# Optimization experiments

Measured on AMD Instinct MI355X. Metric: run time of the kernel, lower is better.

Reference implementation:

```python
import jax, jax.numpy as jnp
import numpy as np

B, D, K = 64, 8732, 81
RATIO = 1.0

def setup_inputs() -> dict:
    key = jax.random.key(0)
    k1, k2, k3, k4 = jax.random.split(key, 4)
    return {
        'loc_preds': jax.random.normal(k1, (B, D, 4), dtype=jnp.float32),
        'loc_targets': jax.random.normal(k2, (B, D, 4), dtype=jnp.float32),
        'conf_preds': jax.random.normal(k3, (B, D, K), dtype=jnp.float32),
        'conf_targets': jax.random.randint(k4, (B, D), 0, K, dtype=jnp.int32),
    }

def reference(loc_preds, loc_targets, conf_preds, conf_targets):
    b, d, k = conf_preds.shape
    pos = conf_targets > 0                                  # [B, D] bool
    num_matched = jnp.sum(pos).astype(conf_preds.dtype)     # scalar (python float in torch)
    num_matched = jax.lax.stop_gradient(num_matched)

    # --- localization smooth-L1 over positive boxes only ---
    z = jnp.abs(loc_preds - loc_targets)
    sl1 = jnp.where(z < 1.0, 0.5 * z * z, z - 0.5)          # [B, D, 4]
    loc_loss = jnp.sum(sl1 * pos[..., None].astype(sl1.dtype))

    # --- per-box CE (custom: GLOBAL max for stability), detached, for mining ---
    x = conf_preds.reshape(-1, k)                           # [B*D, K]
    y = conf_targets.reshape(-1)                            # [B*D]
    xmax = jnp.max(x)                                       # x.data.max() in torch (global scalar)
    lse = jnp.log(jnp.sum(jnp.exp(x - xmax), axis=1)) + xmax
    ce_mine = lse - jnp.take_along_axis(x, y[:, None].astype(jnp.int32), axis=1)[:, 0]
    conf_loss_mat = jax.lax.stop_gradient(ce_mine).reshape(b, d)

    # --- hard negative mining: double argsort rank trick ---
    cl = jnp.where(pos, 0.0, conf_loss_mat)                 # conf_loss[pos] = 0
    idx = jnp.argsort(-cl, axis=1)                          # descending sort indices
    rank = jnp.argsort(idx, axis=1)                         # rank of each box
    num_pos = jnp.sum(pos, axis=1, keepdims=True).astype(jnp.float32)   # [B,1]
    num_neg = jnp.minimum(3.0 * RATIO * num_pos, float(d - 1))          # clamp max=D-1
    neg = rank.astype(jnp.float32) < num_neg                # [B, D] bool

    # --- final confidence loss: standard CE summed over pos | neg ---
    sel = (pos | neg).reshape(-1)                           # [B*D]
    logp = jax.nn.log_softmax(x, axis=1)
    ce = -jnp.take_along_axis(logp, y[:, None].astype(jnp.int32), axis=1)[:, 0]
    conf_loss = jnp.sum(jnp.where(sel, ce, 0.0))

    loc_loss = loc_loss / num_matched
    conf_loss = conf_loss / num_matched
    return (loc_loss + conf_loss, conf_loss, loc_loss)
```

## Files before the change

### kernel.cpp

```cpp
#include <hip/hip_runtime.h>
#include <math.h>

constexpr int BB = 64;
constexpr int DD = 8732;
constexpr int KK = 81;
constexpr int SL = 137;
constexpr int NCHUNK = BB * SL;
constexpr int NPART = NCHUNK;
constexpr int NBLKS = 2048;

typedef float f4 __attribute__((ext_vector_type(4)));

__device__ inline float smooth_l1(float d) {
    float z = fabsf(d);
    return z < 1.0f ? 0.5f * z * z : z - 0.5f;
}

__global__ void __launch_bounds__(256) fused_kernel(
    const f4* __restrict__ lp, const f4* __restrict__ lt,
    const float* __restrict__ cp, const int* __restrict__ ct,
    int* __restrict__ cnt_part, float* __restrict__ ce_part,
    float* __restrict__ loc_part)
{
    int tid = threadIdx.x;
    int q = tid & 3, grp = tid >> 2;
    int lane = tid & 63, wid = tid >> 6;
    __shared__ float s_l[4], s_e[4];
    __shared__ int   s_c[4];

    for (int c = blockIdx.x; c < NCHUNK; c += NBLKS) {
        int row = c / SL, sl = c - row * SL;
        int bir = sl * 64 + grp;
        float ce_c = 0.0f, locs = 0.0f;
        int cc = 0;
        if (bir < DD) {
            size_t g = (size_t)row * DD + bir;
            const float* rowp = cp + g * KK;
            const f4* r4 = (const f4*)rowp;
            f4 f[5];
            #pragma unroll
            for (int t = 0; t < 5; ++t) f[t] = r4[q + 4 * t];

            float s = 0.0f;
            #pragma unroll
            for (int t = 0; t < 5; ++t)
                s += __expf(f[t].x) + __expf(f[t].y)
                   + __expf(f[t].z) + __expf(f[t].w);
            if (q == 0) s += __expf(rowp[80]);
            s += __shfl_xor(s, 1);
            s += __shfl_xor(s, 2);

            int y = ct[g];
            float xv = rowp[y];
            if (q == 0) ce_c = __logf(s) - xv;
            if (q == 1 && y > 0) {
                cc = 1;
                f4 a = lp[g], b = lt[g];
                locs = smooth_l1(a.x - b.x) + smooth_l1(a.y - b.y)
                     + smooth_l1(a.z - b.z) + smooth_l1(a.w - b.w);
            }
        }
        for (int o = 32; o; o >>= 1) {
            locs += __shfl_down(locs, o);
            ce_c += __shfl_down(ce_c, o);
            cc   += __shfl_down(cc, o);
        }
        if (c != blockIdx.x) __syncthreads();
        if (lane == 0) { s_l[wid] = locs; s_e[wid] = ce_c; s_c[wid] = cc; }
        __syncthreads();
        if (tid == 0) {
            loc_part[c] = s_l[0] + s_l[1] + s_l[2] + s_l[3];
            ce_part[c]  = s_e[0] + s_e[1] + s_e[2] + s_e[3];
            cnt_part[c] = s_c[0] + s_c[1] + s_c[2] + s_c[3];
        }
    }
}

__global__ void __launch_bounds__(1024) finish_kernel(
    const int* __restrict__ cnt_part, const float* __restrict__ ce_part,
    const float* __restrict__ loc_part, const float* __restrict__ cp,
    const int* __restrict__ ct, float* __restrict__ out)
{
    __shared__ int s_np[BB];
    __shared__ double s_ce[BB];
    __shared__ double s_l[16], s_n[16], s_fs[16];
    __shared__ double s_conf;
    __shared__ int s_fb[BB], s_nfb;
    __shared__ float cl[DD];

    int tid = threadIdx.x;
    int lane = tid & 63, wid = tid >> 6;
    int row = tid >> 4, sub = tid & 15;

    int np = 0; double ces = 0.0;
    for (int s = sub; s < SL; s += 16) {
        int idx = row * SL + s;
        np += cnt_part[idx];
        ces += (double)ce_part[idx];
    }
    for (int o = 8; o; o >>= 1) { np += __shfl_down(np, o); ces += __shfl_down(ces, o); }
    if (sub == 0) { s_np[row] = np; s_ce[row] = ces; }

    double l = 0.0, n = 0.0;
    for (int j = tid; j < NPART; j += 1024) {
        l += (double)loc_part[j];
        n += (double)cnt_part[j];
    }
    for (int o = 32; o; o >>= 1) { l += __shfl_down(l, o); n += __shfl_down(n, o); }
    if (lane == 0) { s_l[wid] = l; s_n[wid] = n; }
    __syncthreads();

    if (tid == 0) {
        double conf = 0.0; int nfb = 0;
        for (int r = 0; r < BB; ++r) {
            float numneg = fminf(3.0f * (float)s_np[r], (float)(DD - 1));
            int M = DD - s_np[r];
            if ((float)M <= numneg) conf += s_ce[r];
            else s_fb[nfb++] = r;
        }
        s_conf = conf; s_nfb = nfb;
    }
    __syncthreads();

    for (int fi = 0; fi < s_nfb; ++fi) {
        int r = s_fb[fi];
        float numneg = fminf(3.0f * (float)s_np[r], (float)(DD - 1));
        const int* ctr = ct + r * DD;
        const float* base = cp + (size_t)r * DD * KK;
        double sum = 0.0;
        for (int i = tid; i < DD; i += 1024) {
            const float* rowp = base + (size_t)i * KK;
            float m = -INFINITY;
            for (int k = 0; k < KK; ++k) m = fmaxf(m, rowp[k]);
            float s = 0.0f;
            for (int k = 0; k < KK; ++k) s += __expf(rowp[k] - m);
            float cei = __logf(s) + m - rowp[ctr[i]];
            if (ctr[i] > 0) { sum += (double)cei; cl[i] = 0.0f; }
            else cl[i] = cei;
        }
        __syncthreads();
        for (int i = tid; i < DD; i += 1024) {
            if (ctr[i] > 0) continue;
            float ci = cl[i];
            int rk = 0;
            for (int j = 0; j < DD; j++) {
                float cj = cl[j];
                rk += (cj > ci || (cj == ci && j < i)) ? 1 : 0;
            }
            if ((float)rk < numneg) sum += (double)ci;
        }
        for (int o = 32; o; o >>= 1) sum += __shfl_down(sum, o);
        if (lane == 0) s_fs[wid] = sum;
        __syncthreads();
        if (tid == 0) {
            double t = 0.0;
            for (int k = 0; k < 16; ++k) t += s_fs[k];
            s_conf += t;
        }
        __syncthreads();
    }

    if (tid == 0) {
        double L = 0.0, N = 0.0;
        for (int k = 0; k < 16; ++k) { L += s_l[k]; N += s_n[k]; }
        double C = s_conf;
        out[0] = (float)(L / N + C / N);
        out[1] = (float)(C / N);
        out[2] = (float)(L / N);
    }
}

extern "C" void kernel_launch(void* const* d_in, const int* in_sizes, int n_in,
                              void* d_out, int out_size, void* d_ws, size_t ws_size,
                              hipStream_t stream) {
    const f4* lp = (const f4*)d_in[0];
    const f4* lt = (const f4*)d_in[1];
    const float* cp = (const float*)d_in[2];
    const int* ct = (const int*)d_in[3];
    float* out = (float*)d_out;

    char* w = (char*)d_ws;
    int*   cnt_part = (int*)w;
    float* loc_part = (float*)(w + 35072);
    float* ce_part  = (float*)(w + 70144);

    fused_kernel<<<NBLKS, 256, 0, stream>>>(lp, lt, cp, ct,
                                            cnt_part, ce_part, loc_part);
    finish_kernel<<<1, 1024, 0, stream>>>(cnt_part, ce_part, loc_part, cp, ct, out);
}
```

Before: 51.68 us.

## Stream conf_preds as flat 64-byte lines per thread with shared-memory box reduction

The main kernel now treats each block's 192 boxes as a contiguous span of floats. Each of up to 972 threads loads one 16-float aligned line with four vector loads, computes exps, and atomically adds partial sums into per-box shared accumulators, also picking out the target logit. This replaces the prior 4-threads-per-box strided row access, which issued misaligned loads (81-float rows) plus a scalar tail and gather, with fully coalesced aligned loads. Because blocks can straddle batch rows, per-block partials are split into two segments that the finish kernel folds into per-row sums with shared atomics. The cost is extra LDS atomics, a float instead of double per-row CE accumulation, and a large 1024-thread block size.

```diff
diff --git a/kernel.cpp b/kernel.cpp
--- a/kernel.cpp
+++ b/kernel.cpp
@@ -4,10 +4,10 @@
 constexpr int BB = 64;
 constexpr int DD = 8732;
 constexpr int KK = 81;
-constexpr int SL = 137;
-constexpr int NCHUNK = BB * SL;
-constexpr int NPART = NCHUNK;
-constexpr int NBLKS = 2048;
+constexpr int NBOX = BB * DD;
+constexpr int BXB = 192;
+constexpr int DWB = BXB * KK;
+constexpr int NBLK = (NBOX + BXB - 1) / BXB;
 
 typedef float f4 __attribute__((ext_vector_type(4)));
 
@@ -16,95 +16,115 @@
     return z < 1.0f ? 0.5f * z * z : z - 0.5f;
 }
 
-__global__ void __launch_bounds__(256) fused_kernel(
+__global__ void __launch_bounds__(1024) fused_kernel(
     const f4* __restrict__ lp, const f4* __restrict__ lt,
     const float* __restrict__ cp, const int* __restrict__ ct,
-    int* __restrict__ cnt_part, float* __restrict__ ce_part,
-    float* __restrict__ loc_part)
+    int* __restrict__ cntA, float* __restrict__ ceA,
+    int* __restrict__ cntB, float* __restrict__ ceB,
+    float* __restrict__ locP)
 {
-    int tid = threadIdx.x;
-    int q = tid & 3, grp = tid >> 2;
+    __shared__ float bsum[BXB];
+    __shared__ float bxv[BXB];
+    __shared__ int   bct[BXB];
+    __shared__ float reA[16], reB[16], rl[16];
+    __shared__ int   rcA[16], rcB[16];
+
+    int tid = threadIdx.x, blk = blockIdx.x;
+    int g0 = blk * BXB;
+    int nb = min(BXB, NBOX - g0);
+    int nlines = nb * KK / 16;
+
+    if (tid < nb) { bct[tid] = ct[g0 + tid]; bsum[tid] = 0.0f; }
+    __syncthreads();
+
+    if (tid < nlines) {
+        size_t d0 = (size_t)blk * DWB + (size_t)tid * 16;
+        const f4* p = (const f4*)(cp + d0);
+        f4 a0 = p[0], a1 = p[1], a2 = p[2], a3 = p[3];
+        int lb  = (tid * 16) / KK;
+        int rem = tid * 16 - lb * KK;
+        int k = KK - rem; if (k > 16) k = 16;
+        float v[16] = { a0.x, a0.y, a0.z, a0.w, a1.x, a1.y, a1.z, a1.w,
+                        a2.x, a2.y, a2.z, a2.w, a3.x, a3.y, a3.z, a3.w };
+        int jt0 = bct[lb] - rem;
+        int jt1 = 1000;
+        if (k < 16) jt1 = k + bct[lb + 1];
+        float xv0 = 0.0f, xv1 = 0.0f, s0 = 0.0f, s1 = 0.0f;
+        #pragma unroll
+        for (int j = 0; j < 16; ++j) {
+            float vj = v[j];
+            if (j == jt0) xv0 = vj;
+            if (j == jt1) xv1 = vj;
+            float e = __expf(vj);
+            if (j < k) s0 += e; else s1 += e;
+        }
+        atomicAdd(&bsum[lb], s0);
+        if ((unsigned)jt0 < 16u) bxv[lb] = xv0;
+        if (k < 16) {
+            atomicAdd(&bsum[lb + 1], s1);
+            if (jt1 < 16) bxv[lb + 1] = xv1;
+        }
+    }
+    __syncthreads();
+
+    float ce = 0.0f, loc = 0.0f; int cnt = 0, seg = 0;
+    if (tid < nb) {
+        int g = g0 + tid;
+        int y = bct[tid];
+        ce = __logf(bsum[tid]) - bxv[tid];
+        seg = (g / DD) - (g0 / DD);
+        if (y > 0) {
+            cnt = 1;
+            f4 A = lp[g], Bv = lt[g];
+            loc = smooth_l1(A.x - Bv.x) + smooth_l1(A.y - Bv.y)
+                + smooth_l1(A.z - Bv.z) + smooth_l1(A.w - Bv.w);
+        }
+    }
+    float ceAv = seg ? 0.0f : ce, ceBv = seg ? ce : 0.0f;
+    int   cAv  = seg ? 0 : cnt,  cBv  = seg ? cnt : 0;
+    for (int o = 32; o; o >>= 1) {
+        ceAv += __shfl_down(ceAv, o); ceBv += __shfl_down(ceBv, o);
+        cAv  += __shfl_down(cAv,  o); cBv  += __shfl_down(cBv,  o);
+        loc  += __shfl_down(loc,  o);
+    }
     int lane = tid & 63, wid = tid >> 6;
-    __shared__ float s_l[4], s_e[4];
-    __shared__ int   s_c[4];
-
-    for (int c = blockIdx.x; c < NCHUNK; c += NBLKS) {
-        int row = c / SL, sl = c - row * SL;
-        int bir = sl * 64 + grp;
-        float ce_c = 0.0f, locs = 0.0f;
-        int cc = 0;
-        if (bir < DD) {
-            size_t g = (size_t)row * DD + bir;
-            const float* rowp = cp + g * KK;
-            const f4* r4 = (const f4*)rowp;
-            f4 f[5];
-            #pragma unroll
-            for (int t = 0; t < 5; ++t) f[t] = r4[q + 4 * t];
-
-            float s = 0.0f;
-            #pragma unroll
-            for (int t = 0; t < 5; ++t)
-                s += __expf(f[t].x) + __expf(f[t].y)
-                   + __expf(f[t].z) + __expf(f[t].w);
-            if (q == 0) s += __expf(rowp[80]);
-            s += __shfl_xor(s, 1);
-            s += __shfl_xor(s, 2);
-
-            int y = ct[g];
-            float xv = rowp[y];
-            if (q == 0) ce_c = __logf(s) - xv;
-            if (q == 1 && y > 0) {
-                cc = 1;
-                f4 a = lp[g], b = lt[g];
-                locs = smooth_l1(a.x - b.x) + smooth_l1(a.y - b.y)
-                     + smooth_l1(a.z - b.z) + smooth_l1(a.w - b.w);
-            }
-        }
-        for (int o = 32; o; o >>= 1) {
-            locs += __shfl_down(locs, o);
-            ce_c += __shfl_down(ce_c, o);
-            cc   += __shfl_down(cc, o);
-        }
-        if (c != blockIdx.x) __syncthreads();
-        if (lane == 0) { s_l[wid] = locs; s_e[wid] = ce_c; s_c[wid] = cc; }
-        __syncthreads();
-        if (tid == 0) {
-            loc_part[c] = s_l[0] + s_l[1] + s_l[2] + s_l[3];
-            ce_part[c]  = s_e[0] + s_e[1] + s_e[2] + s_e[3];
-            cnt_part[c] = s_c[0] + s_c[1] + s_c[2] + s_c[3];
-        }
+    if (lane == 0) { reA[wid]=ceAv; reB[wid]=ceBv; rcA[wid]=cAv; rcB[wid]=cBv; rl[wid]=loc; }
+    __syncthreads();
+    if (tid == 0) {
+        float eA = 0, eB = 0, L = 0; int cA = 0, cB = 0;
+        #pragma unroll
+        for (int w = 0; w < 16; ++w) { eA+=reA[w]; eB+=reB[w]; cA+=rcA[w]; cB+=rcB[w]; L+=rl[w]; }
+        ceA[blk] = eA; ceB[blk] = eB; cntA[blk] = cA; cntB[blk] = cB; locP[blk] = L;
     }
 }
 
 __global__ void __launch_bounds__(1024) finish_kernel(
-    const int* __restrict__ cnt_part, const float* __restrict__ ce_part,
-    const float* __restrict__ loc_part, const float* __restrict__ cp,
+    const int* __restrict__ cntA, const float* __restrict__ ceA,
+    const int* __restrict__ cntB, const float* __restrict__ ceB,
+    const float* __restrict__ locP, const float* __restrict__ cp,
     const int* __restrict__ ct, float* __restrict__ out)
 {
-    __shared__ int s_np[BB];
-    __shared__ double s_ce[BB];
+    __shared__ int   s_np[BB];
+    __shared__ float s_cef[BB];
     __shared__ double s_l[16], s_n[16], s_fs[16];
     __shared__ double s_conf;
     __shared__ int s_fb[BB], s_nfb;
     __shared__ float cl[DD];
 
-    int tid = threadIdx.x;
-    int lane = tid & 63, wid = tid >> 6;
-    int row = tid >> 4, sub = tid & 15;
-
-    int np = 0; double ces = 0.0;
-    for (int s = sub; s < SL; s += 16) {
-        int idx = row * SL + s;
-        np += cnt_part[idx];
-        ces += (double)ce_part[idx];
-    }
-    for (int o = 8; o; o >>= 1) { np += __shfl_down(np, o); ces += __shfl_down(ces, o); }
-    if (sub == 0) { s_np[row] = np; s_ce[row] = ces; }
+    int tid = threadIdx.x, lane = tid & 63, wid = tid >> 6;
+    if (tid < BB) { s_np[tid] = 0; s_cef[tid] = 0.0f; }
+    __syncthreads();
 
     double l = 0.0, n = 0.0;
-    for (int j = tid; j < NPART; j += 1024) {
-        l += (double)loc_part[j];
-        n += (double)cnt_part[j];
+    for (int e = tid; e < NBLK; e += 1024) {
+        int rA = (e * BXB) / DD;
+        int ca = cntA[e], cb = cntB[e];
+        float ea = ceA[e], eb = ceB[e];
+        atomicAdd(&s_np[rA], ca);
+        atomicAdd(&s_cef[rA], ea);
+        if (rA + 1 < BB) { atomicAdd(&s_np[rA + 1], cb); atomicAdd(&s_cef[rA + 1], eb); }
+        l += (double)locP[e];
+        n += (double)(ca + cb);
     }
     for (int o = 32; o; o >>= 1) { l += __shfl_down(l, o); n += __shfl_down(n, o); }
     if (lane == 0) { s_l[wid] = l; s_n[wid] = n; }
@@ -115,7 +135,7 @@
         for (int r = 0; r < BB; ++r) {
             float numneg = fminf(3.0f * (float)s_np[r], (float)(DD - 1));
             int M = DD - s_np[r];
-            if ((float)M <= numneg) conf += s_ce[r];
+            if ((float)M <= numneg) conf += (double)s_cef[r];
             else s_fb[nfb++] = r;
         }
         s_conf = conf; s_nfb = nfb;
@@ -131,9 +151,9 @@
         for (int i = tid; i < DD; i += 1024) {
             const float* rowp = base + (size_t)i * KK;
             float m = -INFINITY;
-            for (int k = 0; k < KK; ++k) m = fmaxf(m, rowp[k]);
+            for (int kk = 0; kk < KK; ++kk) m = fmaxf(m, rowp[kk]);
             float s = 0.0f;
-            for (int k = 0; k < KK; ++k) s += __expf(rowp[k] - m);
+            for (int kk = 0; kk < KK; ++kk) s += __expf(rowp[kk] - m);
             float cei = __logf(s) + m - rowp[ctr[i]];
             if (ctr[i] > 0) { sum += (double)cei; cl[i] = 0.0f; }
             else cl[i] = cei;
@@ -154,7 +174,7 @@
         __syncthreads();
         if (tid == 0) {
             double t = 0.0;
-            for (int k = 0; k < 16; ++k) t += s_fs[k];
+            for (int kk = 0; kk < 16; ++kk) t += s_fs[kk];
             s_conf += t;
         }
         __syncthreads();
@@ -162,7 +182,7 @@
 
     if (tid == 0) {
         double L = 0.0, N = 0.0;
-        for (int k = 0; k < 16; ++k) { L += s_l[k]; N += s_n[k]; }
+        for (int kk = 0; kk < 16; ++kk) { L += s_l[kk]; N += s_n[kk]; }
         double C = s_conf;
         out[0] = (float)(L / N + C / N);
         out[1] = (float)(C / N);
@@ -180,11 +200,14 @@
     float* out = (float*)d_out;
 
     char* w = (char*)d_ws;
-    int*   cnt_part = (int*)w;
-    float* loc_part = (float*)(w + 35072);
-    float* ce_part  = (float*)(w + 70144);
-
-    fused_kernel<<<NBLKS, 256, 0, stream>>>(lp, lt, cp, ct,
-                                            cnt_part, ce_part, loc_part);
-    finish_kernel<<<1, 1024, 0, stream>>>(cnt_part, ce_part, loc_part, cp, ct, out);
-}
+    int*   cntA = (int*)w;
+    int*   cntB = (int*)(w + 12288);
+    float* ceA  = (float*)(w + 24576);
+    float* ceB  = (float*)(w + 36864);
+    float* locP = (float*)(w + 49152);
+
+    fused_kernel<<<NBLK, 1024, 0, stream>>>(lp, lt, cp, ct,
+                                            cntA, ceA, cntB, ceB, locP);
+    finish_kernel<<<1, 1024, 0, stream>>>(cntA, ceA, cntB, ceB, locP,
+                                          cp, ct, out);
+}
```

Result: slower. 73.27 us (+41.8%).
